# Kernel tuning notes

Measured on AMD Instinct MI355X. Metric: run time of the kernel, lower is better.

## Reference

```python
import jax, jax.numpy as jnp
import numpy as np

LATENT_DIM = 512
ASSET_DIM = 8192


def setup_inputs() -> dict:
    key = jax.random.key(0)
    ks = jax.random.split(key, 7)
    d = LATENT_DIM
    s = 1.0 / np.sqrt(d)  # torch Linear default init scale (uniform bound)
    z = jax.random.normal(ks[0], (ASSET_DIM, d), dtype=jnp.float32)
    Wq = jax.random.uniform(ks[1], (d, d), jnp.float32, -s, s)
    Wk = jax.random.uniform(ks[2], (d, d), jnp.float32, -s, s)
    Wv = jax.random.uniform(ks[3], (d, d), jnp.float32, -s, s)
    bq = jax.random.uniform(ks[4], (d,), jnp.float32, -s, s)
    bk = jax.random.uniform(ks[5], (d,), jnp.float32, -s, s)
    bv = jax.random.uniform(ks[6], (d,), jnp.float32, -s, s)
    return {"z": z, "Wq": Wq, "bq": bq, "Wk": Wk, "bk": bk, "Wv": Wv, "bv": bv}


def reference(z, Wq, bq, Wk, bk, Wv, bv):
    # z: (N, D). Single-head self-attention over assets.
    d = z.shape[-1]
    scale = d ** (-0.5)
    q = z @ Wq.T + bq          # (N, D)
    k = z @ Wk.T + bk          # (N, D)
    v = z @ Wv.T + bv          # (N, D)
    scores = jnp.einsum('nd,md->nm', q, k) * scale   # (N, N)
    attn = jax.nn.softmax(scores, axis=-1)
    # Original does attn[:, :, None] * v[None] then sum(dim=1); identical math:
    h = attn @ v               # (N, D)
    return h
```

## Files before the change

kernel.cpp:

```cpp
#include <hip/hip_runtime.h>
#include <hip/hip_bf16.h>
#include <stdint.h>

#define D 512
#define N 8192

typedef __attribute__((ext_vector_type(8))) short short8;
typedef __attribute__((ext_vector_type(4))) float f32x4;

static __device__ __forceinline__ unsigned short f2bf(float f) {
  unsigned int u = __builtin_bit_cast(unsigned int, f);
  u += 0x7fffu + ((u >> 16) & 1u);
  return (unsigned short)(u >> 16);
}
static __device__ __forceinline__ float bf2f(unsigned short s) {
  unsigned int u = ((unsigned int)s) << 16;
  return __builtin_bit_cast(float, u);
}

typedef const __attribute__((address_space(1))) unsigned int* gas_ptr;
typedef __attribute__((address_space(3))) unsigned int* las_ptr;
static __device__ __forceinline__ void gload_lds16(const void* g, void* l) {
  __builtin_amdgcn_global_load_lds((gas_ptr)g, (las_ptr)l, 16, 0, 0);
}

__global__ void cast_z_k(const float* __restrict__ z, unsigned short* __restrict__ zb) {
  int i = blockIdx.x * 256 + threadIdx.x;
  const int n4 = N * D / 4;
  for (; i < n4; i += gridDim.x * 256) {
    float4 v = ((const float4*)z)[i];
    ushort4 o = { f2bf(v.x), f2bf(v.y), f2bf(v.z), f2bf(v.w) };
    ((ushort4*)zb)[i] = o;
  }
}

__global__ void cast_w_k(const float* __restrict__ Wq, const float* __restrict__ Wk,
                         const float* __restrict__ Wv, const float* __restrict__ bq,
                         const float* __restrict__ bk, const float* __restrict__ bv,
                         unsigned short* __restrict__ wb, float* __restrict__ bqkv) {
  const float scale = 0.044194173824159216f;
  int i = blockIdx.x * 256 + threadIdx.x;
  const int per = D * D / 4;
  if (i < 3 * per) {
    int sec = i / per;
    int w4 = i - sec * per;
    const float* W = sec == 0 ? Wq : (sec == 1 ? Wk : Wv);
    float s = sec == 0 ? scale : 1.0f;
    float4 v = ((const float4*)W)[w4];
    ushort4 o = { f2bf(v.x * s), f2bf(v.y * s), f2bf(v.z * s), f2bf(v.w * s) };
    ((ushort4*)wb)[sec * per + w4] = o;
  }
  if (i < 3 * D) {
    int sec = i >> 9, j = i & (D - 1);
    const float* b = sec == 0 ? bq : (sec == 1 ? bk : bv);
    bqkv[i] = b[j] * (sec == 0 ? scale : 1.0f);
  }
}

#define BM 128
#define BN 128
#define BK 64

template <int EPI>
__global__ __launch_bounds__(256) void gemm_nt(
    const unsigned short* __restrict__ A, int lda,
    const unsigned short* __restrict__ B, int ldb,
    int K, int tiles_n,
    const float* __restrict__ bias,
    unsigned short* __restrict__ o0, unsigned short* __restrict__ o1,
    unsigned short* __restrict__ o2,
    float* __restrict__ lpart, float* __restrict__ outF) {
  __shared__ unsigned short Ash[2][BM * BK];
  __shared__ unsigned short Bsh[2][BN * BK];

  const int t = threadIdx.x;
  const int w = t >> 6, lane = t & 63;
  const int bid = blockIdx.x, nwg = gridDim.x;
  const int cpx = nwg >> 3;
  const int swz = (bid & 7) * cpx + (bid >> 3);
  const int tm = swz / tiles_n, tn = swz - tm * tiles_n;
  const int row0 = tm * BM, col0 = tn * BN;

  const int srow = t >> 3;
  const int scol = ((t & 7) ^ ((t >> 3) & 7)) * 8;
  const unsigned short* Ab = A + (size_t)(row0 + srow) * lda + scol;
  const unsigned short* Bb = B + (size_t)(col0 + srow) * ldb + scol;
  const int ldsbase = (w * 64) * 8;

  const int l15 = lane & 15, lhi = lane >> 4, lx = lane & 7;
  const int wr = w >> 1, wc = w & 1;
  const int arow = (wr * 64 + l15) * BK;
  const int brow = (wc * 64 + l15) * BK;
  const int ko0 = ((0 + lhi) ^ lx) * 8;
  const int ko1 = ((4 + lhi) ^ lx) * 8;

  f32x4 acc[4][4] = {};

  auto stage = [&](int buf, int k0) {
    const unsigned short* a = Ab + k0;
    const unsigned short* b = Bb + k0;
    unsigned short* la = &Ash[buf][ldsbase];
    unsigned short* lb = &Bsh[buf][ldsbase];
#pragma unroll
    for (int i = 0; i < 4; ++i) {
      gload_lds16(a + (size_t)(i * 32) * lda, la + i * 2048);
      gload_lds16(b + (size_t)(i * 32) * ldb, lb + i * 2048);
    }
  };

  const int NT = K / BK;
  stage(0, 0);
  asm volatile("s_waitcnt vmcnt(0)" ::: "memory");
  __syncthreads();
  int cur = 0;
  for (int kt = 0; kt < NT; ++kt) {
    if (kt + 1 < NT) stage(cur ^ 1, (kt + 1) * BK);
    const unsigned short* As = Ash[cur];
    const unsigned short* Bs = Bsh[cur];
#pragma unroll
    for (int ks = 0; ks < 2; ++ks) {
      const int ko = ks ? ko1 : ko0;
      short8 af[4], bg[4];
#pragma unroll
      for (int rf = 0; rf < 4; ++rf)
        af[rf] = *(const short8*)(As + arow + rf * (16 * BK) + ko);
#pragma unroll
      for (int cf = 0; cf < 4; ++cf)
        bg[cf] = *(const short8*)(Bs + brow + cf * (16 * BK) + ko);
#pragma unroll
      for (int rf = 0; rf < 4; ++rf)
#pragma unroll
        for (int cf = 0; cf < 4; ++cf)
          acc[rf][cf] = __builtin_amdgcn_mfma_f32_16x16x32_bf16(af[rf], bg[cf], acc[rf][cf], 0, 0, 0);
    }
    asm volatile("s_waitcnt vmcnt(0)" ::: "memory");
    __syncthreads();
    cur ^= 1;
  }

  const int r0g = row0 + wr * 64;
  const int c0g = col0 + wc * 64;

  if constexpr (EPI == 0) {
    const int sec = col0 >> 9;
#pragma unroll
    for (int cf = 0; cf < 4; ++cf) {
      const int c = c0g + cf * 16 + l15;
      const int cj = c & (D - 1);
      const float bb = bias[c];
#pragma unroll
      for (int rf = 0; rf < 4; ++rf) {
        const int r = r0g + rf * 16 + lhi * 4;
        f32x4 v = acc[rf][cf];
        if (sec == 0) {
#pragma unroll
          for (int g = 0; g < 4; ++g) o0[(size_t)(r + g) * D + cj] = f2bf(v[g] + bb);
        } else if (sec == 1) {
#pragma unroll
          for (int g = 0; g < 4; ++g) o1[(size_t)(r + g) * D + cj] = f2bf(v[g] + bb);
        } else {
          ushort4 o = { f2bf(v[0] + bb), f2bf(v[1] + bb), f2bf(v[2] + bb), f2bf(v[3] + bb) };
          *(ushort4*)(o2 + (size_t)cj * N + r) = o;
        }
      }
    }
  }

  if constexpr (EPI == 1) {
    float rs[4][4];
#pragma unroll
    for (int rf = 0; rf < 4; ++rf)
#pragma unroll
      for (int g = 0; g < 4; ++g) rs[rf][g] = 0.f;
#pragma unroll
    for (int cf = 0; cf < 4; ++cf) {
      const int c = c0g + cf * 16 + l15;
#pragma unroll
      for (int rf = 0; rf < 4; ++rf) {
        const int r = r0g + rf * 16 + lhi * 4;
        f32x4 v = acc[rf][cf];
#pragma unroll
        for (int g = 0; g < 4; ++g) {
          unsigned short us = f2bf(__expf(v[g]));
          o0[(size_t)(r + g) * N + c] = us;
          rs[rf][g] += bf2f(us);
        }
      }
    }
#pragma unroll
    for (int rf = 0; rf < 4; ++rf)
#pragma unroll
      for (int g = 0; g < 4; ++g) {
        float s = rs[rf][g];
        s += __shfl_xor(s, 1);
        s += __shfl_xor(s, 2);
        s += __shfl_xor(s, 4);
        s += __shfl_xor(s, 8);
        rs[rf][g] = s;
      }
    if (l15 == 0) {
      const int slot = tn * 2 + wc;
#pragma unroll
      for (int rf = 0; rf < 4; ++rf)
#pragma unroll
        for (int g = 0; g < 4; ++g)
          lpart[(size_t)slot * N + r0g + rf * 16 + lhi * 4 + g] = rs[rf][g];
    }
  }

  if constexpr (EPI == 2) {
    __shared__ float linv[BM];
    {
      const int rr = t >> 1, half = t & 1;
      float s = 0.f;
      for (int i = 0; i < 64; ++i)
        s += lpart[(size_t)(half * 64 + i) * N + row0 + rr];
      s += __shfl_xor(s, 1);
      if (half == 0) linv[rr] = 1.0f / s;
    }
    __syncthreads();
#pragma unroll
    for (int cf = 0; cf < 4; ++cf) {
      const int c = c0g + cf * 16 + l15;
#pragma unroll
      for (int rf = 0; rf < 4; ++rf) {
        const int rl = wr * 64 + rf * 16 + lhi * 4;
        f32x4 v = acc[rf][cf];
#pragma unroll
        for (int g = 0; g < 4; ++g)
          outF[(size_t)(row0 + rl + g) * D + c] = v[g] * linv[rl + g];
      }
    }
  }
}

extern "C" void kernel_launch(void* const* d_in, const int* in_sizes, int n_in,
                              void* d_out, int out_size, void* d_ws, size_t ws_size,
                              hipStream_t stream) {
  const float* z  = (const float*)d_in[0];
  const float* Wq = (const float*)d_in[1];
  const float* bq = (const float*)d_in[2];
  const float* Wk = (const float*)d_in[3];
  const float* bk = (const float*)d_in[4];
  const float* Wv = (const float*)d_in[5];
  const float* bv = (const float*)d_in[6];
  float* out = (float*)d_out;

  char* ws = (char*)d_ws;
  unsigned short* zb = (unsigned short*)(ws + 0);
  unsigned short* qb = (unsigned short*)(ws + 8388608);
  unsigned short* kb = (unsigned short*)(ws + 16777216);
  unsigned short* vT = (unsigned short*)(ws + 25165824);
  unsigned short* wb = (unsigned short*)(ws + 33554432);
  float* bqkv       = (float*)(ws + 35127296);
  float* lpart      = (float*)(ws + 35133440);
  unsigned short* P = (unsigned short*)(ws + 39327744);

  cast_z_k<<<dim3(2048), dim3(256), 0, stream>>>(z, zb);
  cast_w_k<<<dim3(768), dim3(256), 0, stream>>>(Wq, Wk, Wv, bq, bk, bv, wb, bqkv);

  gemm_nt<0><<<dim3(64 * 12), dim3(256), 0, stream>>>(
      zb, D, wb, D, D, 12, bqkv, qb, kb, vT, (float*)nullptr, (float*)nullptr);

  gemm_nt<1><<<dim3(64 * 64), dim3(256), 0, stream>>>(
      qb, D, kb, D, D, 64, (const float*)nullptr, P, (unsigned short*)nullptr,
      (unsigned short*)nullptr, lpart, (float*)nullptr);

  gemm_nt<2><<<dim3(64 * 4), dim3(256), 0, stream>>>(
      P, N, vT, N, N, 4, (const float*)nullptr, (unsigned short*)nullptr,
      (unsigned short*)nullptr, (unsigned short*)nullptr, lpart, out);
}
```

Before: 282.8 us.

## Split-K the attn@V GEMM three ways with bf16 partials and a reduce kernel

```diff
diff --git a/kernel.cpp b/kernel.cpp
--- a/kernel.cpp
+++ b/kernel.cpp
@@ -69,7 +69,7 @@
     const float* __restrict__ bias,
     unsigned short* __restrict__ o0, unsigned short* __restrict__ o1,
     unsigned short* __restrict__ o2,
-    float* __restrict__ lpart, float* __restrict__ outF) {
+    float* __restrict__ lpart) {
   __shared__ unsigned short Ash[2][BM * BK];
   __shared__ unsigned short Bsh[2][BN * BK];
 
@@ -78,7 +78,18 @@
   const int bid = blockIdx.x, nwg = gridDim.x;
   const int cpx = nwg >> 3;
   const int swz = (bid & 7) * cpx + (bid >> 3);
-  const int tm = swz / tiles_n, tn = swz - tm * tiles_n;
+  int tm, tn, kt0 = 0, nkt = K / BK, sidx = 0;
+  if constexpr (EPI == 3) {
+    sidx = swz >> 8;
+    const int tile = swz & 255;
+    tm = tile >> 2;
+    tn = tile & 3;
+    kt0 = sidx * 43;
+    nkt = (sidx < 2) ? 43 : 42;
+  } else {
+    tm = swz / tiles_n;
+    tn = swz - tm * tiles_n;
+  }
   const int row0 = tm * BM, col0 = tn * BN;
 
   const int srow = t >> 3;
@@ -108,13 +119,12 @@
     }
   };
 
-  const int NT = K / BK;
-  stage(0, 0);
+  stage(0, kt0 * BK);
   asm volatile("s_waitcnt vmcnt(0)" ::: "memory");
   __syncthreads();
   int cur = 0;
-  for (int kt = 0; kt < NT; ++kt) {
-    if (kt + 1 < NT) stage(cur ^ 1, (kt + 1) * BK);
+  for (int kt = 0; kt < nkt; ++kt) {
+    if (kt + 1 < nkt) stage(cur ^ 1, (kt0 + kt + 1) * BK);
     const unsigned short* As = Ash[cur];
     const unsigned short* Bs = Bsh[cur];
 #pragma unroll
@@ -208,30 +218,44 @@
     }
   }
 
-  if constexpr (EPI == 2) {
-    __shared__ float linv[BM];
-    {
-      const int rr = t >> 1, half = t & 1;
-      float s = 0.f;
-      for (int i = 0; i < 64; ++i)
-        s += lpart[(size_t)(half * 64 + i) * N + row0 + rr];
-      s += __shfl_xor(s, 1);
-      if (half == 0) linv[rr] = 1.0f / s;
-    }
-    __syncthreads();
+  if constexpr (EPI == 3) {
+    unsigned short* op = o0 + (size_t)sidx * ((size_t)N * D);
 #pragma unroll
     for (int cf = 0; cf < 4; ++cf) {
       const int c = c0g + cf * 16 + l15;
 #pragma unroll
       for (int rf = 0; rf < 4; ++rf) {
-        const int rl = wr * 64 + rf * 16 + lhi * 4;
+        const int r = r0g + rf * 16 + lhi * 4;
         f32x4 v = acc[rf][cf];
 #pragma unroll
-        for (int g = 0; g < 4; ++g)
-          outF[(size_t)(row0 + rl + g) * D + c] = v[g] * linv[rl + g];
+        for (int g = 0; g < 4; ++g) op[(size_t)(r + g) * D + c] = f2bf(v[g]);
       }
     }
   }
+}
+
+__global__ void linv_k(const float* __restrict__ lpart, float* __restrict__ linv) {
+  const int m = blockIdx.x * 256 + threadIdx.x;
+  float s = 0.f;
+  for (int i = 0; i < 128; ++i) s += lpart[(size_t)i * N + m];
+  linv[m] = 1.0f / s;
+}
+
+__global__ void reduce_k(const unsigned short* __restrict__ Opart,
+                         const float* __restrict__ linv, float* __restrict__ out) {
+  const int i = blockIdx.x * 256 + threadIdx.x;
+  const int m = i >> 7;
+  const float li = linv[m];
+  const size_t nd = (size_t)N * D;
+  ushort4 a = ((const ushort4*)Opart)[i];
+  ushort4 b = ((const ushort4*)(Opart + nd))[i];
+  ushort4 c = ((const ushort4*)(Opart + 2 * nd))[i];
+  float4 o;
+  o.x = (bf2f(a.x) + bf2f(b.x) + bf2f(c.x)) * li;
+  o.y = (bf2f(a.y) + bf2f(b.y) + bf2f(c.y)) * li;
+  o.z = (bf2f(a.z) + bf2f(b.z) + bf2f(c.z)) * li;
+  o.w = (bf2f(a.w) + bf2f(b.w) + bf2f(c.w)) * li;
+  ((float4*)out)[i] = o;
 }
 
 extern "C" void kernel_launch(void* const* d_in, const int* in_sizes, int n_in,
@@ -252,21 +276,27 @@
   unsigned short* kb = (unsigned short*)(ws + 16777216);
   unsigned short* vT = (unsigned short*)(ws + 25165824);
   unsigned short* wb = (unsigned short*)(ws + 33554432);
+  float* linv       = (float*)(ws + 33554432);
   float* bqkv       = (float*)(ws + 35127296);
   float* lpart      = (float*)(ws + 35133440);
   unsigned short* P = (unsigned short*)(ws + 39327744);
+  unsigned short* Opart = (unsigned short*)(ws + 0);
 
   cast_z_k<<<dim3(2048), dim3(256), 0, stream>>>(z, zb);
   cast_w_k<<<dim3(768), dim3(256), 0, stream>>>(Wq, Wk, Wv, bq, bk, bv, wb, bqkv);
 
   gemm_nt<0><<<dim3(64 * 12), dim3(256), 0, stream>>>(
-      zb, D, wb, D, D, 12, bqkv, qb, kb, vT, (float*)nullptr, (float*)nullptr);
+      zb, D, wb, D, D, 12, bqkv, qb, kb, vT, (float*)nullptr);
 
   gemm_nt<1><<<dim3(64 * 64), dim3(256), 0, stream>>>(
       qb, D, kb, D, D, 64, (const float*)nullptr, P, (unsigned short*)nullptr,
-      (unsigned short*)nullptr, lpart, (float*)nullptr);
-
-  gemm_nt<2><<<dim3(64 * 4), dim3(256), 0, stream>>>(
-      P, N, vT, N, N, 4, (const float*)nullptr, (unsigned short*)nullptr,
-      (unsigned short*)nullptr, (unsigned short*)nullptr, lpart, out);
-}
+      (unsigned short*)nullptr, lpart);
+
+  linv_k<<<dim3(32), dim3(256), 0, stream>>>(lpart, linv);
+
+  gemm_nt<3><<<dim3(768), dim3(256), 0, stream>>>(
+      P, N, vT, N, N, 4, (const float*)nullptr, Opart, (unsigned short*)nullptr,
+      (unsigned short*)nullptr, (float*)nullptr);
+
+  reduce_k<<<dim3(4096), dim3(256), 0, stream>>>(Opart, linv, out);
+}
```

New measurement: 269.4 us. 1.05x faster.
